# Kernel optimization log

Measured on AMD Instinct MI355X. Metric: run time of the kernel, lower is better.

Reference implementation:

```python
import jax, jax.numpy as jnp
import numpy as np

B, N, C_IN = 8, 2048, 64
NUM_TERMS, NUM_CHANNELS = 3, 64
LN_EPS = 1e-5


def setup_inputs() -> dict:
    key = jax.random.key(0)
    k1, k2, k3 = jax.random.split(key, 3)
    A = jax.random.normal(k1, (B, N, N), dtype=jnp.float32) / jnp.sqrt(N).astype(jnp.float32)
    X = jax.random.normal(k2, (B, N, C_IN), dtype=jnp.float32)
    # xavier_uniform on h of shape [num_terms+1, num_channels, num_nodes]
    fan_in, fan_out = NUM_CHANNELS, N
    bound = float(np.sqrt(6.0 / (fan_in + fan_out)))
    h = jax.random.uniform(k3, (NUM_TERMS + 1, NUM_CHANNELS, N), dtype=jnp.float32,
                           minval=-bound, maxval=bound)
    gamma = jnp.ones((NUM_CHANNELS,), dtype=jnp.float32)
    beta = jnp.zeros((NUM_CHANNELS,), dtype=jnp.float32)
    return {"A": A, "X": X, "h": h, "gamma": gamma, "beta": beta}


def reference(A, X, h, gamma, beta):
    # Original loops compute: Y[b,n,c] = sum_i h[i,c,n] * (A^i @ sum_ch X[...,ch])[b,n]
    num_terms = h.shape[0] - 1
    Xs = X.sum(axis=-1)  # [B, N] -- inner channel loop collapses to a sum

    def step(p, _):
        p_next = jnp.einsum('bmn,bn->bm', A, p)  # A^i @ Xs
        return p_next, p_next

    _, Ps = jax.lax.scan(step, Xs, None, length=num_terms)  # [T, B, N]
    P = jnp.concatenate([Xs[None], Ps], axis=0)  # [T+1, B, N], P[0] = I @ Xs

    Y = jnp.einsum('icn,ibn->bnc', h, P)  # [B, N, C]

    mean = Y.mean(axis=-1, keepdims=True)
    var = Y.var(axis=-1, keepdims=True)
    Yn = (Y - mean) * jax.lax.rsqrt(var + LN_EPS) * gamma + beta
    return jnp.tanh(Yn)
```

## Files before the change

### kernel.cpp

```cpp
#include <hip/hip_runtime.h>
#include <hip/hip_bf16.h>
#include <math.h>

#define BB 8
#define NN 2048
#define C_IN 64
#define NCH 64
#define NTERMS 3
#define LN_EPS 1e-5f

__global__ void xsum_kernel(const float* __restrict__ X, float* __restrict__ Xs) {
    int row  = (blockIdx.x * blockDim.x + threadIdx.x) >> 6;
    int lane = threadIdx.x & 63;
    float v = X[(size_t)row * C_IN + lane];
    #pragma unroll
    for (int off = 32; off > 0; off >>= 1)
        v += __shfl_down(v, off, 64);
    if (lane == 0) Xs[row] = v;
}

__global__ __launch_bounds__(256, 8) void matvec_kernel(
        const float* __restrict__ A,
        const float* __restrict__ pin,
        float* __restrict__ pout) {
    __shared__ float p[NN];
    const int b = blockIdx.y;

    const float4* pin4 = (const float4*)(pin + (size_t)b * NN);
    float4* p4 = (float4*)p;
    p4[threadIdx.x]       = pin4[threadIdx.x];
    p4[threadIdx.x + 256] = pin4[threadIdx.x + 256];
    __syncthreads();

    const int wave = threadIdx.x >> 6;
    const int lane = threadIdx.x & 63;
    const int m    = blockIdx.x * 4 + wave;

    const float4* Ar = (const float4*)(A + (size_t)b * NN * NN + (size_t)m * NN);

    float4 x[8];
    #pragma unroll
    for (int j = 0; j < 8; ++j)
        x[j] = Ar[j * 64 + lane];

    float acc = 0.f;
    #pragma unroll
    for (int j = 0; j < 8; ++j) {
        float4 pv = p4[j * 64 + lane];
        acc += x[j].x * pv.x + x[j].y * pv.y + x[j].z * pv.z + x[j].w * pv.w;
    }

    #pragma unroll
    for (int off = 32; off > 0; off >>= 1)
        acc += __shfl_down(acc, off, 64);
    if (lane == 0) pout[(size_t)b * NN + m] = acc;
}

__global__ __launch_bounds__(512) void combine_kernel(
        const float* __restrict__ h,
        const float* __restrict__ P,
        const float* __restrict__ gamma,
        const float* __restrict__ beta,
        float* __restrict__ out) {
    const int n    = blockIdx.x;
    const int b    = threadIdx.x >> 6;
    const int lane = threadIdx.x & 63;
    const int idx  = b * NN + n;

    const float p0 = P[0 * BB * NN + idx];
    const float p1 = P[1 * BB * NN + idx];
    const float p2 = P[2 * BB * NN + idx];
    const float p3 = P[3 * BB * NN + idx];

    float y = h[(size_t)(0 * NCH + lane) * NN + n] * p0
            + h[(size_t)(1 * NCH + lane) * NN + n] * p1
            + h[(size_t)(2 * NCH + lane) * NN + n] * p2
            + h[(size_t)(3 * NCH + lane) * NN + n] * p3;

    float s = y;
    #pragma unroll
    for (int off = 32; off > 0; off >>= 1)
        s += __shfl_xor(s, off, 64);
    const float mean = s * (1.f / NCH);

    float d = y - mean;
    float vs = d * d;
    #pragma unroll
    for (int off = 32; off > 0; off >>= 1)
        vs += __shfl_xor(vs, off, 64);
    const float rstd = rsqrtf(vs * (1.f / NCH) + LN_EPS);

    out[(size_t)idx * NCH + lane] = tanhf(d * rstd * gamma[lane] + beta[lane]);
}

extern "C" void kernel_launch(void* const* d_in, const int* in_sizes, int n_in,
                              void* d_out, int out_size, void* d_ws, size_t ws_size,
                              hipStream_t stream) {
    const float* A     = (const float*)d_in[0];
    const float* X     = (const float*)d_in[1];
    const float* h     = (const float*)d_in[2];
    const float* gamma = (const float*)d_in[3];
    const float* beta  = (const float*)d_in[4];
    float* out = (float*)d_out;

    float* P = (float*)d_ws;

    {
        int rows = BB * NN;
        xsum_kernel<<<rows / 4, 256, 0, stream>>>(X, P);
    }

    dim3 mv_grid(NN / 4, BB);
    for (int i = 1; i <= NTERMS; ++i) {
        matvec_kernel<<<mv_grid, 256, 0, stream>>>(
            A, P + (size_t)(i - 1) * BB * NN, P + (size_t)i * BB * NN);
    }

    combine_kernel<<<NN, 512, 0, stream>>>(h, P, gamma, beta, out);
}
```

Before: 254.2 us.

## Convert A to fp16 during first matvec and reuse it for later terms

The first power-iteration matvec reads A in fp32 and also writes an fp16 copy into workspace. The remaining matvecs read this half-size copy and accumulate in fp32. This cuts the HBM bytes read in the later passes at the cost of an extra 64 MB write and fp16 rounding of A. The p vector is now loaded straight from global memory rather than staged in shared memory.

Result: no change. 249.3 us (-1.9%).

```diff
diff --git a/kernel.cpp b/kernel.cpp
--- a/kernel.cpp
+++ b/kernel.cpp
@@ -1,5 +1,6 @@
 #include <hip/hip_runtime.h>
 #include <hip/hip_bf16.h>
+#include <hip/hip_fp16.h>
 #include <math.h>
 
 #define BB 8
@@ -19,35 +20,76 @@
     if (lane == 0) Xs[row] = v;
 }
 
-__global__ __launch_bounds__(256, 8) void matvec_kernel(
+__global__ __launch_bounds__(256, 4) void matvec_cvt_kernel(
         const float* __restrict__ A,
         const float* __restrict__ pin,
-        float* __restrict__ pout) {
-    __shared__ float p[NN];
-    const int b = blockIdx.y;
-
-    const float4* pin4 = (const float4*)(pin + (size_t)b * NN);
-    float4* p4 = (float4*)p;
-    p4[threadIdx.x]       = pin4[threadIdx.x];
-    p4[threadIdx.x + 256] = pin4[threadIdx.x + 256];
-    __syncthreads();
-
+        float* __restrict__ pout,
+        __half* __restrict__ A16) {
+    const int b    = blockIdx.y;
     const int wave = threadIdx.x >> 6;
     const int lane = threadIdx.x & 63;
     const int m    = blockIdx.x * 4 + wave;
 
-    const float4* Ar = (const float4*)(A + (size_t)b * NN * NN + (size_t)m * NN);
+    const float4* pin4 = (const float4*)(pin + (size_t)b * NN);
+    const float4* Ar   = (const float4*)(A + (size_t)b * NN * NN + (size_t)m * NN);
 
-    float4 x[8];
+    float4 x[8], pr[8];
     #pragma unroll
-    for (int j = 0; j < 8; ++j)
-        x[j] = Ar[j * 64 + lane];
+    for (int j = 0; j < 8; ++j) x[j]  = Ar[j * 64 + lane];
+    #pragma unroll
+    for (int j = 0; j < 8; ++j) pr[j] = pin4[j * 64 + lane];
 
     float acc = 0.f;
     #pragma unroll
+    for (int j = 0; j < 8; ++j)
+        acc += x[j].x * pr[j].x + x[j].y * pr[j].y + x[j].z * pr[j].z + x[j].w * pr[j].w;
+
+    float2* A16r = (float2*)(A16 + (size_t)b * NN * NN + (size_t)m * NN);
+    #pragma unroll
     for (int j = 0; j < 8; ++j) {
-        float4 pv = p4[j * 64 + lane];
-        acc += x[j].x * pv.x + x[j].y * pv.y + x[j].z * pv.z + x[j].w * pv.w;
+        union { float2 f2; __half2 h2[2]; } u;
+        u.h2[0] = __floats2half2_rn(x[j].x, x[j].y);
+        u.h2[1] = __floats2half2_rn(x[j].z, x[j].w);
+        A16r[j * 64 + lane] = u.f2;
+    }
+
+    #pragma unroll
+    for (int off = 32; off > 0; off >>= 1)
+        acc += __shfl_down(acc, off, 64);
+    if (lane == 0) pout[(size_t)b * NN + m] = acc;
+}
+
+__global__ __launch_bounds__(256, 4) void matvec16_kernel(
+        const __half* __restrict__ A16,
+        const float* __restrict__ pin,
+        float* __restrict__ pout) {
+    const int b    = blockIdx.y;
+    const int wave = threadIdx.x >> 6;
+    const int lane = threadIdx.x & 63;
+    const int m    = blockIdx.x * 4 + wave;
+
+    const float4* pin4 = (const float4*)(pin + (size_t)b * NN);
+    const float4* Ar   = (const float4*)(A16 + (size_t)b * NN * NN + (size_t)m * NN);
+
+    float4 xr[4], pa[4], pb[4];
+    #pragma unroll
+    for (int j = 0; j < 4; ++j) xr[j] = Ar[j * 64 + lane];
+    #pragma unroll
+    for (int j = 0; j < 4; ++j) {
+        pa[j] = pin4[2 * (j * 64 + lane)];
+        pb[j] = pin4[2 * (j * 64 + lane) + 1];
+    }
+
+    float acc = 0.f;
+    #pragma unroll
+    for (int j = 0; j < 4; ++j) {
+        const __half2* hx = (const __half2*)&xr[j];
+        float2 f0 = __half22float2(hx[0]);
+        float2 f1 = __half22float2(hx[1]);
+        float2 f2 = __half22float2(hx[2]);
+        float2 f3 = __half22float2(hx[3]);
+        acc += f0.x * pa[j].x + f0.y * pa[j].y + f1.x * pa[j].z + f1.y * pa[j].w
+             + f2.x * pb[j].x + f2.y * pb[j].y + f3.x * pb[j].z + f3.y * pb[j].w;
     }
 
     #pragma unroll
@@ -103,17 +145,17 @@
     const float* beta  = (const float*)d_in[4];
     float* out = (float*)d_out;
 
-    float* P = (float*)d_ws;
+    float*  P   = (float*)d_ws;
+    __half* A16 = (__half*)((char*)d_ws + (1u << 20));
 
-    {
-        int rows = BB * NN;
-        xsum_kernel<<<rows / 4, 256, 0, stream>>>(X, P);
-    }
+    xsum_kernel<<<(BB * NN) / 4, 256, 0, stream>>>(X, P);
 
     dim3 mv_grid(NN / 4, BB);
-    for (int i = 1; i <= NTERMS; ++i) {
-        matvec_kernel<<<mv_grid, 256, 0, stream>>>(
-            A, P + (size_t)(i - 1) * BB * NN, P + (size_t)i * BB * NN);
+    matvec_cvt_kernel<<<mv_grid, 256, 0, stream>>>(A, P, P + BB * NN, A16);
+
+    for (int i = 2; i <= NTERMS; ++i) {
+        matvec16_kernel<<<mv_grid, 256, 0, stream>>>(
+            A16, P + (size_t)(i - 1) * BB * NN, P + (size_t)i * BB * NN);
     }
 
     combine_kernel<<<NN, 512, 0, stream>>>(h, P, gamma, beta, out);
```
